# Optimization experiments

Measured on AMD Instinct MI355X. Metric: run time of the kernel, lower is better.

The kernel has to match this reference:

```python
import jax, jax.numpy as jnp
import numpy as np

HIDDEN = 2048
INTER = 8192
RETRIEVAL = 128
NUM_EXPERTS = 4096
NUM_KEYS = 64  # sqrt(NUM_EXPERTS)
TOP_K = 8
B, S = 4, 2048


def setup_inputs() -> dict:
    key = jax.random.key(0)
    ks = jax.random.split(key, 8)
    sc = 0.02
    return {
        "hidden_states": jax.random.normal(ks[0], (B, S, HIDDEN), jnp.float32),
        "W_q": jax.random.normal(ks[1], (HIDDEN, RETRIEVAL), jnp.float32) * sc,
        "keys": jax.random.normal(ks[2], (2, RETRIEVAL // 2, NUM_KEYS), jnp.float32) * sc,
        "down_embed": jax.random.normal(ks[3], (NUM_EXPERTS, HIDDEN), jnp.float32) * sc,
        "up_embed": jax.random.normal(ks[4], (NUM_EXPERTS, HIDDEN), jnp.float32) * sc,
        "gate_w": jax.random.normal(ks[5], (HIDDEN, INTER), jnp.float32) * sc,
        "up_w": jax.random.normal(ks[6], (HIDDEN, INTER), jnp.float32) * sc,
        "down_w": jax.random.normal(ks[7], (INTER, HIDDEN), jnp.float32) * sc,
    }


def reference(hidden_states, W_q, keys, down_embed, up_embed, gate_w, up_w, down_w):
    b, s, h = hidden_states.shape
    n = b * s
    # product-key routing (faithful to the source's view(2, N, -1) reshape)
    queries = (hidden_states @ W_q).reshape(2, n, RETRIEVAL // 2)  # [2, N, rd/2]
    routing = jnp.einsum('tnd,tdk->tnk', queries, keys)            # [2, N, num_keys]
    scores2, idx2 = jax.lax.top_k(routing, TOP_K)                  # [2, N, k]
    sx, sy = scores2[0], scores2[1]
    ix, iy = idx2[0], idx2[1]
    all_scores = (sx[:, :, None] + sy[:, None, :]).reshape(n, TOP_K * TOP_K)
    all_idx = (ix[:, :, None] * NUM_KEYS + iy[:, None, :]).reshape(n, TOP_K * TOP_K)
    scores, pk = jax.lax.top_k(all_scores, TOP_K)                  # [N, k]
    indices = jnp.take_along_axis(all_idx, pk, axis=-1)            # [N, k]
    # expert embedding gather + per-token tiny matmuls
    de = down_embed[indices]                                       # [N, k, H]
    ue = up_embed[indices]                                         # [N, k, H]
    x = hidden_states.reshape(n, h)
    ew = jnp.einsum('nh,nkh->nk', x, de)                           # [N, k]
    ew = jax.nn.silu(ew) * jax.nn.softmax(scores, axis=-1)
    experts_states = jnp.einsum('nk,nkh->nh', ew, ue).reshape(b, s, h)
    # dense SwiGLU MLP branch
    mlp = (jax.nn.silu(x @ gate_w) * (x @ up_w)) @ down_w
    return mlp.reshape(b, s, h) + experts_states
```

## Files before the change

### kernel.cpp

```cpp
#include <hip/hip_runtime.h>
#include <cstdint>
#include <cstddef>

#define HIDDEN 2048
#define INTER 8192
#define NTOK 8192
#define RET 128
#define NKEYS 64
#define TOPK 8

typedef __bf16 bf16_t;
typedef bf16_t bf16x8 __attribute__((ext_vector_type(8)));
typedef float floatx4 __attribute__((ext_vector_type(4)));

__device__ inline unsigned short f2bf(float f) {
  union { float f; unsigned u; } v; v.f = f;
  unsigned r = v.u + 0x7FFFu + ((v.u >> 16) & 1u);
  return (unsigned short)(r >> 16);
}
__device__ inline float bf2f(unsigned short s) {
  union { unsigned u; float f; } v; v.u = ((unsigned)s) << 16;
  return v.f;
}

__device__ inline void gld_lds16(unsigned short* lds, const unsigned short* g) {
  auto* l3 = reinterpret_cast<__attribute__((address_space(3))) unsigned int*>(
      reinterpret_cast<uintptr_t>(lds));
  auto* g1 = reinterpret_cast<const __attribute__((address_space(1))) unsigned int*>(
      reinterpret_cast<uintptr_t>(g));
  __builtin_amdgcn_global_load_lds(g1, l3, 16, 0, 0);
}

__device__ inline void xcd_map(int gx, int gy, int& bx, int& by) {
  if ((gx & 7) != 0) return;
  int lin = by * gx + bx;
  int W = gx >> 3;
  int xcd = lin & 7;
  int j = lin >> 3;
  int r = j / W, c = j % W;
  if (r & 1) c = W - 1 - c;
  bx = xcd * W + c;
  by = r;
}

__global__ __launch_bounds__(256) void cvt_bf16(const float* __restrict__ in,
                                                unsigned short* __restrict__ out,
                                                int count4) {
  for (int i = blockIdx.x * blockDim.x + threadIdx.x; i < count4;
       i += gridDim.x * blockDim.x) {
    float4 v = reinterpret_cast<const float4*>(in)[i];
    ushort4 o;
    o.x = f2bf(v.x); o.y = f2bf(v.y); o.z = f2bf(v.z); o.w = f2bf(v.w);
    reinterpret_cast<ushort4*>(out)[i] = o;
  }
}

__global__ __launch_bounds__(256) void transpose_cvt(const float* __restrict__ in,
                                                     unsigned short* __restrict__ out,
                                                     int R, int C) {
  __shared__ float tile[32][33];
  int c0 = blockIdx.x * 32, r0 = blockIdx.y * 32;
  int tx = threadIdx.x, ty = threadIdx.y;
#pragma unroll
  for (int it = 0; it < 4; ++it)
    tile[ty + it * 8][tx] = in[(size_t)(r0 + ty + it * 8) * C + c0 + tx];
  __syncthreads();
#pragma unroll
  for (int it = 0; it < 4; ++it)
    out[(size_t)(c0 + ty + it * 8) * R + r0 + tx] = f2bf(tile[tx][ty + it * 8]);
}

enum { EPI_F32 = 0, EPI_ADDF32 = 3 };

template <int MODE>
__global__ __launch_bounds__(256) void gemm_bt(const unsigned short* __restrict__ A,
                                               const unsigned short* __restrict__ B,
                                               float* __restrict__ Cf,
                                               int M, int N, int K) {
  __shared__ unsigned short As[128 * 64];
  __shared__ unsigned short Bs[128 * 64];
  const int tid = threadIdx.x;
  const int lane = tid & 63, wid = tid >> 6;
  const int wm = wid >> 1, wn = wid & 1;
  int bx = blockIdx.x, by = blockIdx.y;
  xcd_map(gridDim.x, gridDim.y, bx, by);
  const int m0 = by * 128, n0 = bx * 128;
  const int lr = lane & 15, q = lane >> 4;
  const int swz = lr & 7;

  floatx4 acc[4][4];
#pragma unroll
  for (int i = 0; i < 4; ++i)
#pragma unroll
    for (int j = 0; j < 4; ++j) acc[i][j] = (floatx4){0.f, 0.f, 0.f, 0.f};

  for (int k0 = 0; k0 < K; k0 += 64) {
#pragma unroll
    for (int s = 0; s < 4; ++s) {
      int c = s * 256 + wid * 64 + lane;
      int row = c >> 3, cc = (c & 7) ^ (row & 7);
      gld_lds16(&As[(s * 256 + wid * 64) * 8],
                A + (size_t)(m0 + row) * K + k0 + cc * 8);
      gld_lds16(&Bs[(s * 256 + wid * 64) * 8],
                B + (size_t)(n0 + row) * K + k0 + cc * 8);
    }
    __syncthreads();
#pragma unroll
    for (int kc = 0; kc < 2; ++kc) {
      const int coff = ((kc * 4 + q) ^ swz) * 8;
      bf16x8 af[4], bfv[4];
#pragma unroll
      for (int t = 0; t < 4; ++t) {
        af[t] = *reinterpret_cast<const bf16x8*>(
            &As[(wm * 64 + t * 16 + lr) * 64 + coff]);
        bfv[t] = *reinterpret_cast<const bf16x8*>(
            &Bs[(wn * 64 + t * 16 + lr) * 64 + coff]);
      }
#pragma unroll
      for (int i = 0; i < 4; ++i)
#pragma unroll
        for (int j = 0; j < 4; ++j)
          acc[i][j] = __builtin_amdgcn_mfma_f32_16x16x32_bf16(af[i], bfv[j],
                                                              acc[i][j], 0, 0, 0);
    }
    __syncthreads();
  }

#pragma unroll
  for (int i = 0; i < 4; ++i) {
    int rbase = m0 + wm * 64 + i * 16 + q * 4;
#pragma unroll
    for (int j = 0; j < 4; ++j) {
      int col = n0 + wn * 64 + j * 16 + lr;
#pragma unroll
      for (int r = 0; r < 4; ++r) {
        size_t idx = (size_t)(rbase + r) * N + col;
        float v = acc[i][j][r];
        if (MODE == EPI_F32) Cf[idx] = v;
        else Cf[idx] = v + Cf[idx];
      }
    }
  }
}

__global__ __launch_bounds__(256, 2) void gemm_gateup(
    const unsigned short* __restrict__ A, const unsigned short* __restrict__ Bg,
    const unsigned short* __restrict__ Bu, unsigned short* __restrict__ H,
    int M, int N, int K) {
  __shared__ unsigned short As[128 * 64];
  __shared__ unsigned short Bgs[128 * 64];
  __shared__ unsigned short Bus[128 * 64];
  const int tid = threadIdx.x;
  const int lane = tid & 63, wid = tid >> 6;
  const int wm = wid >> 1, wn = wid & 1;
  int bx = blockIdx.x, by = blockIdx.y;
  xcd_map(gridDim.x, gridDim.y, bx, by);
  const int m0 = by * 128, n0 = bx * 128;
  const int lr = lane & 15, q = lane >> 4;
  const int swz = lr & 7;

  floatx4 accg[4][4], accu[4][4];
#pragma unroll
  for (int i = 0; i < 4; ++i)
#pragma unroll
    for (int j = 0; j < 4; ++j) {
      accg[i][j] = (floatx4){0.f, 0.f, 0.f, 0.f};
      accu[i][j] = (floatx4){0.f, 0.f, 0.f, 0.f};
    }

  for (int k0 = 0; k0 < K; k0 += 64) {
#pragma unroll
    for (int s = 0; s < 4; ++s) {
      int c = s * 256 + wid * 64 + lane;
      int row = c >> 3, cc = (c & 7) ^ (row & 7);
      size_t arow = (size_t)(m0 + row) * K + k0 + cc * 8;
      size_t brow = (size_t)(n0 + row) * K + k0 + cc * 8;
      gld_lds16(&As[(s * 256 + wid * 64) * 8], A + arow);
      gld_lds16(&Bgs[(s * 256 + wid * 64) * 8], Bg + brow);
      gld_lds16(&Bus[(s * 256 + wid * 64) * 8], Bu + brow);
    }
    __syncthreads();
#pragma unroll
    for (int kc = 0; kc < 2; ++kc) {
      const int coff = ((kc * 4 + q) ^ swz) * 8;
      bf16x8 af[4], bgf[4], buf[4];
#pragma unroll
      for (int t = 0; t < 4; ++t) {
        af[t] = *reinterpret_cast<const bf16x8*>(
            &As[(wm * 64 + t * 16 + lr) * 64 + coff]);
        bgf[t] = *reinterpret_cast<const bf16x8*>(
            &Bgs[(wn * 64 + t * 16 + lr) * 64 + coff]);
        buf[t] = *reinterpret_cast<const bf16x8*>(
            &Bus[(wn * 64 + t * 16 + lr) * 64 + coff]);
      }
#pragma unroll
      for (int i = 0; i < 4; ++i)
#pragma unroll
        for (int j = 0; j < 4; ++j) {
          accg[i][j] = __builtin_amdgcn_mfma_f32_16x16x32_bf16(af[i], bgf[j],
                                                               accg[i][j], 0, 0, 0);
          accu[i][j] = __builtin_amdgcn_mfma_f32_16x16x32_bf16(af[i], buf[j],
                                                               accu[i][j], 0, 0, 0);
        }
    }
    __syncthreads();
  }

#pragma unroll
  for (int i = 0; i < 4; ++i) {
    int rbase = m0 + wm * 64 + i * 16 + q * 4;
#pragma unroll
    for (int j = 0; j < 4; ++j) {
      int col = n0 + wn * 64 + j * 16 + lr;
#pragma unroll
      for (int r = 0; r < 4; ++r) {
        float g = accg[i][j][r];
        float h = (g / (1.f + __expf(-g))) * accu[i][j][r];
        H[(size_t)(rbase + r) * N + col] = f2bf(h);
      }
    }
  }
}

__global__ __launch_bounds__(256) void routing_kernel(const float* __restrict__ Q,
                                                      const float* __restrict__ keys,
                                                      int* __restrict__ topi,
                                                      float* __restrict__ topw) {
  __shared__ float k0s[64 * 64];
  __shared__ float k1s[64 * 64];
  for (int i = threadIdx.x; i < 64 * 64; i += 256) {
    k0s[i] = keys[i];
    k1s[i] = keys[64 * 64 + i];
  }
  __syncthreads();
  const int lane = threadIdx.x & 63, wid = threadIdx.x >> 6;
  const int gw = blockIdx.x * 4 + wid;
  const float NEG = -__builtin_inff();

  for (int n = gw; n < NTOK; n += 1024) {
    int cbase = (n & 1) * 64;
    float qx = Q[(size_t)(n >> 1) * RET + cbase + lane];
    float qy = Q[(size_t)(NTOK / 2 + (n >> 1)) * RET + cbase + lane];
    float rx = 0.f, ry = 0.f;
#pragma unroll 8
    for (int d = 0; d < 64; ++d) {
      rx += __shfl(qx, d) * k0s[d * 64 + lane];
      ry += __shfl(qy, d) * k1s[d * 64 + lane];
    }
    float mvx = rx, mvy = ry;
    float keptx = 0.f, kepty = 0.f;
    int keptix = 0, keptiy = 0;
#pragma unroll
    for (int a = 0; a < 8; ++a) {
      float v = mvx; int ii = lane;
#pragma unroll
      for (int off = 32; off; off >>= 1) {
        float ov = __shfl_xor(v, off); int oi = __shfl_xor(ii, off);
        if (ov > v || (ov == v && oi < ii)) { v = ov; ii = oi; }
      }
      if (lane == a) { keptx = v; keptix = ii; }
      if (lane == ii) mvx = NEG;
      float w = mvy; int jj = lane;
#pragma unroll
      for (int off = 32; off; off >>= 1) {
        float ow = __shfl_xor(w, off); int oj = __shfl_xor(jj, off);
        if (ow > w || (ow == w && oj < jj)) { w = ow; jj = oj; }
      }
      if (lane == a) { kepty = w; keptiy = jj; }
      if (lane == jj) mvy = NEG;
    }
    float sa = __shfl(keptx, lane >> 3), sb = __shfl(kepty, lane & 7);
    int ia = __shfl(keptix, lane >> 3), ib = __shfl(keptiy, lane & 7);
    float mv = sa + sb;
    int pe = ia * NKEYS + ib;
    float maxs = 0.f, denom = 0.f, kw = 0.f;
    int ke = 0;
#pragma unroll
    for (int a = 0; a < 8; ++a) {
      float v = mv; int pos = lane; int e = pe;
#pragma unroll
      for (int off = 32; off; off >>= 1) {
        float ov = __shfl_xor(v, off);
        int opos = __shfl_xor(pos, off);
        int oe = __shfl_xor(e, off);
        if (ov > v || (ov == v && opos < pos)) { v = ov; pos = opos; e = oe; }
      }
      if (a == 0) maxs = v;
      denom += __expf(v - maxs);
      if (lane == a) { kw = __expf(v - maxs); ke = e; }
      if (lane == pos) mv = NEG;
    }
    if (lane < 8) {
      topw[(size_t)n * 8 + lane] = kw / denom;
      topi[(size_t)n * 8 + lane] = ke;
    }
  }
}

__global__ __launch_bounds__(256) void expert_kernel(const float* __restrict__ X,
                                                     const float* __restrict__ de,
                                                     const float* __restrict__ ue,
                                                     const int* __restrict__ topi,
                                                     const float* __restrict__ topw,
                                                     float* __restrict__ out) {
  const int n = blockIdx.x, t = threadIdx.x;
  __shared__ float red[4];
  __shared__ float coef_s;
  __shared__ int eidx[8];
  __shared__ float ewt[8];
  if (t < 8) {
    eidx[t] = topi[(size_t)n * 8 + t];
    ewt[t] = topw[(size_t)n * 8 + t];
  }
  const float* x = X + (size_t)n * HIDDEN + t * 8;
  float4 x0 = *(const float4*)x, x1 = *(const float4*)(x + 4);
  float a0 = 0, a1 = 0, a2 = 0, a3 = 0, a4 = 0, a5 = 0, a6 = 0, a7 = 0;
  __syncthreads();
#pragma unroll
  for (int k = 0; k < 8; ++k) {
    const float* dr = de + (size_t)eidx[k] * HIDDEN + t * 8;
    float4 d0 = *(const float4*)dr, d1 = *(const float4*)(dr + 4);
    float p = x0.x * d0.x + x0.y * d0.y + x0.z * d0.z + x0.w * d0.w +
              x1.x * d1.x + x1.y * d1.y + x1.z * d1.z + x1.w * d1.w;
#pragma unroll
    for (int off = 32; off; off >>= 1) p += __shfl_xor(p, off);
    if ((t & 63) == 0) red[t >> 6] = p;
    __syncthreads();
    if (t == 0) {
      float s = red[0] + red[1] + red[2] + red[3];
      coef_s = (s / (1.f + expf(-s))) * ewt[k];
    }
    __syncthreads();
    float c = coef_s;
    const float* ur = ue + (size_t)eidx[k] * HIDDEN + t * 8;
    float4 u0 = *(const float4*)ur, u1 = *(const float4*)(ur + 4);
    a0 += c * u0.x; a1 += c * u0.y; a2 += c * u0.z; a3 += c * u0.w;
    a4 += c * u1.x; a5 += c * u1.y; a6 += c * u1.z; a7 += c * u1.w;
  }
  float* op = out + (size_t)n * HIDDEN + t * 8;
  *(float4*)op = make_float4(a0, a1, a2, a3);
  *(float4*)(op + 4) = make_float4(a4, a5, a6, a7);
}

extern "C" void kernel_launch(void* const* d_in, const int* in_sizes, int n_in,
                              void* d_out, int out_size, void* d_ws, size_t ws_size,
                              hipStream_t stream) {
  const float* X    = (const float*)d_in[0];
  const float* Wq   = (const float*)d_in[1];
  const float* keys = (const float*)d_in[2];
  const float* de   = (const float*)d_in[3];
  const float* ue   = (const float*)d_in[4];
  const float* Wg   = (const float*)d_in[5];
  const float* Wu   = (const float*)d_in[6];
  const float* Wd   = (const float*)d_in[7];
  float* out = (float*)d_out;

  char* ws = (char*)d_ws;
  size_t o = 0;
  unsigned short* xb  = (unsigned short*)(ws + o); o += (size_t)NTOK * HIDDEN * 2;
  unsigned short* wgt = (unsigned short*)(ws + o); o += (size_t)HIDDEN * INTER * 2;
  unsigned short* wut = (unsigned short*)(ws + o); o += (size_t)HIDDEN * INTER * 2;
  unsigned short* wdt = (unsigned short*)(ws + o); o += (size_t)HIDDEN * INTER * 2;
  unsigned short* hbuf= (unsigned short*)(ws + o); o += (size_t)NTOK * INTER * 2;
  unsigned short* wqt = (unsigned short*)(ws + o); o += (size_t)RET * HIDDEN * 2;
  float* Q            = (float*)(ws + o);          o += (size_t)NTOK * RET * 4;
  int* topi           = (int*)(ws + o);            o += (size_t)NTOK * TOPK * 4;
  float* topw         = (float*)(ws + o);          o += (size_t)NTOK * TOPK * 4;

  cvt_bf16<<<4096, 256, 0, stream>>>(X, xb, NTOK * HIDDEN / 4);
  transpose_cvt<<<dim3(INTER / 32, HIDDEN / 32), dim3(32, 8), 0, stream>>>(Wg, wgt, HIDDEN, INTER);
  transpose_cvt<<<dim3(INTER / 32, HIDDEN / 32), dim3(32, 8), 0, stream>>>(Wu, wut, HIDDEN, INTER);
  transpose_cvt<<<dim3(HIDDEN / 32, INTER / 32), dim3(32, 8), 0, stream>>>(Wd, wdt, INTER, HIDDEN);
  transpose_cvt<<<dim3(RET / 32, HIDDEN / 32), dim3(32, 8), 0, stream>>>(Wq, wqt, HIDDEN, RET);

  gemm_bt<EPI_F32><<<dim3(1, NTOK / 128), 256, 0, stream>>>(xb, wqt, Q,
                                                            NTOK, RET, HIDDEN);
  routing_kernel<<<256, 256, 0, stream>>>(Q, keys, topi, topw);
  expert_kernel<<<NTOK, 256, 0, stream>>>(X, de, ue, topi, topw, out);

  gemm_gateup<<<dim3(INTER / 128, NTOK / 128), 256, 0, stream>>>(
      xb, wgt, wut, hbuf, NTOK, INTER, HIDDEN);
  gemm_bt<EPI_ADDF32><<<dim3(HIDDEN / 128, NTOK / 128), 256, 0, stream>>>(
      hbuf, wdt, out, NTOK, HIDDEN, INTER);
}
```

Measured before the change: 1.573 ms.

## Replace big GEMMs with 256-tile multi-stage pipelined kernels and batch expert reductions

Replaces the gate/up and down-projection GEMMs with 512-thread kernels that use 256-row tiles, a 4-buffer LDS ring with loads issued three tiles ahead, split A/B staging interleaved with MFMA phases, explicit vmcnt waits and raised wave priority during MFMA. This is meant to hide global load latency and raise data reuse per block, at the cost of 128 KB of dynamic LDS and a hand-tuned barrier and wait schedule that is fragile. The expert kernel also batches all eight dot-product reductions into a single barrier instead of two barriers per expert, cutting synchronisation overhead.

```diff
diff --git a/kernel.cpp b/kernel.cpp
--- a/kernel.cpp
+++ b/kernel.cpp
@@ -13,14 +13,26 @@
 typedef bf16_t bf16x8 __attribute__((ext_vector_type(8)));
 typedef float floatx4 __attribute__((ext_vector_type(4)));
 
+#define BARRIER() asm volatile("s_barrier" ::: "memory")
+#define WAIT_LGKM0()                                     \
+  do {                                                   \
+    asm volatile("s_waitcnt lgkmcnt(0)" ::: "memory");   \
+    __builtin_amdgcn_sched_barrier(0);                   \
+  } while (0)
+#define WAIT_VM8() asm volatile("s_waitcnt vmcnt(8)" ::: "memory")
+#define WAIT_VM4() asm volatile("s_waitcnt vmcnt(4)" ::: "memory")
+#define WAIT_VM0() asm volatile("s_waitcnt vmcnt(0)" ::: "memory")
+
+__device__ inline void tile_end_wait(int rem) {
+  if (rem >= 3) WAIT_VM8();
+  else if (rem == 2) WAIT_VM4();
+  else if (rem == 1) WAIT_VM0();
+}
+
 __device__ inline unsigned short f2bf(float f) {
   union { float f; unsigned u; } v; v.f = f;
   unsigned r = v.u + 0x7FFFu + ((v.u >> 16) & 1u);
   return (unsigned short)(r >> 16);
-}
-__device__ inline float bf2f(unsigned short s) {
-  union { unsigned u; float f; } v; v.u = ((unsigned)s) << 16;
-  return v.f;
 }
 
 __device__ inline void gld_lds16(unsigned short* lds, const unsigned short* g) {
@@ -41,6 +53,25 @@
   if (r & 1) c = W - 1 - c;
   bx = xcd * W + c;
   by = r;
+}
+
+__device__ inline void stage_op256(unsigned short* ldsbuf, const unsigned short* g,
+                                   int rows0, int K, int kt, int tid, int wid) {
+#pragma unroll
+  for (int i = 0; i < 2; ++i) {
+    int c = i * 512 + tid;
+    int row = c >> 2;
+    int cc = (c & 3) ^ (row & 3) ^ ((row >> 2) & 3);
+    gld_lds16(ldsbuf + (size_t)(i * 512 + wid * 64) * 8,
+              g + (size_t)(rows0 + row) * K + kt + cc * 8);
+  }
+}
+__device__ inline void stage_op128(unsigned short* ldsbuf, const unsigned short* g,
+                                   int rows0, int K, int kt, int tid, int wid) {
+  int row = tid >> 2;
+  int cc = (tid & 3) ^ (row & 3) ^ ((row >> 2) & 3);
+  gld_lds16(ldsbuf + (size_t)(wid * 64) * 8,
+            g + (size_t)(rows0 + row) * K + kt + cc * 8);
 }
 
 __global__ __launch_bounds__(256) void cvt_bf16(const float* __restrict__ in,
@@ -143,21 +174,123 @@
   }
 }
 
-__global__ __launch_bounds__(256, 2) void gemm_gateup(
-    const unsigned short* __restrict__ A, const unsigned short* __restrict__ Bg,
-    const unsigned short* __restrict__ Bu, unsigned short* __restrict__ H,
-    int M, int N, int K) {
-  __shared__ unsigned short As[128 * 64];
-  __shared__ unsigned short Bgs[128 * 64];
-  __shared__ unsigned short Bus[128 * 64];
+template <int MODE>
+__global__ __launch_bounds__(512, 2) void gemm256(const unsigned short* __restrict__ A,
+                                                  const unsigned short* __restrict__ B,
+                                                  float* __restrict__ Cf,
+                                                  int N, int K) {
+  extern __shared__ unsigned short sm[];
+  const int tid = threadIdx.x;
+  const int lane = tid & 63, wid = tid >> 6;
+  const int wm = wid >> 2, wn = wid & 3;
+  int bx = blockIdx.x, by = blockIdx.y;
+  xcd_map(gridDim.x, gridDim.y, bx, by);
+  const int m0 = by * 256, n0 = bx * 256;
+  const int lr = lane & 15, q = lane >> 4;
+  const int swz = (lr & 3) ^ ((lr >> 2) & 3);
+  const int coff = (q ^ swz) * 8;
+  unsigned short* Abase = sm;
+  unsigned short* Bbase = sm + 32768;
+  const int NT = K >> 5;
+
+  floatx4 acc[8][4];
+#pragma unroll
+  for (int i = 0; i < 8; ++i)
+#pragma unroll
+    for (int j = 0; j < 4; ++j) acc[i][j] = (floatx4){0.f, 0.f, 0.f, 0.f};
+
+#pragma unroll
+  for (int tt = 0; tt < 3; ++tt) {
+    stage_op256(Abase + tt * 8192, A, m0, K, tt * 32, tid, wid);
+    stage_op256(Bbase + tt * 8192, B, n0, K, tt * 32, tid, wid);
+  }
+  WAIT_VM8();
+  BARRIER();
+
+  for (int t = 0; t < NT; ++t) {
+    const int buf = t & 3;
+    const unsigned short* As = Abase + buf * 8192;
+    const unsigned short* Bs = Bbase + buf * 8192;
+    bf16x8 af[4], bfv[4];
+#pragma unroll
+    for (int m = 0; m < 4; ++m)
+      af[m] = *reinterpret_cast<const bf16x8*>(
+          &As[(wm * 128 + m * 16 + lr) * 32 + coff]);
+#pragma unroll
+    for (int n = 0; n < 4; ++n)
+      bfv[n] = *reinterpret_cast<const bf16x8*>(
+          &Bs[(wn * 64 + n * 16 + lr) * 32 + coff]);
+    if (t + 3 < NT)
+      stage_op256(Abase + ((t + 3) & 3) * 8192, A, m0, K, (t + 3) * 32, tid, wid);
+    BARRIER();
+    WAIT_LGKM0();
+    __builtin_amdgcn_s_setprio(1);
+#pragma unroll
+    for (int m = 0; m < 4; ++m)
+#pragma unroll
+      for (int n = 0; n < 4; ++n)
+        acc[m][n] = __builtin_amdgcn_mfma_f32_16x16x32_bf16(af[m], bfv[n],
+                                                            acc[m][n], 0, 0, 0);
+    __builtin_amdgcn_s_setprio(0);
+    __builtin_amdgcn_sched_barrier(0);
+    BARRIER();
+#pragma unroll
+    for (int m = 0; m < 4; ++m)
+      af[m] = *reinterpret_cast<const bf16x8*>(
+          &As[(wm * 128 + (m + 4) * 16 + lr) * 32 + coff]);
+    if (t + 3 < NT)
+      stage_op256(Bbase + ((t + 3) & 3) * 8192, B, n0, K, (t + 3) * 32, tid, wid);
+    BARRIER();
+    WAIT_LGKM0();
+    __builtin_amdgcn_s_setprio(1);
+#pragma unroll
+    for (int m = 0; m < 4; ++m)
+#pragma unroll
+      for (int n = 0; n < 4; ++n)
+        acc[m + 4][n] = __builtin_amdgcn_mfma_f32_16x16x32_bf16(af[m], bfv[n],
+                                                                acc[m + 4][n], 0, 0, 0);
+    __builtin_amdgcn_s_setprio(0);
+    __builtin_amdgcn_sched_barrier(0);
+    tile_end_wait(NT - 1 - t);
+    BARRIER();
+  }
+
+#pragma unroll
+  for (int m = 0; m < 8; ++m) {
+    int rbase = m0 + wm * 128 + m * 16 + q * 4;
+#pragma unroll
+    for (int n = 0; n < 4; ++n) {
+      int col = n0 + wn * 64 + n * 16 + lr;
+#pragma unroll
+      for (int r = 0; r < 4; ++r) {
+        size_t idx = (size_t)(rbase + r) * N + col;
+        float v = acc[m][n][r];
+        if (MODE == EPI_F32) Cf[idx] = v;
+        else Cf[idx] = v + Cf[idx];
+      }
+    }
+  }
+}
+
+__global__ __launch_bounds__(512, 2) void gateup256(const unsigned short* __restrict__ A,
+                                                    const unsigned short* __restrict__ Bg,
+                                                    const unsigned short* __restrict__ Bu,
+                                                    unsigned short* __restrict__ H,
+                                                    int N, int K) {
+  extern __shared__ unsigned short sm[];
   const int tid = threadIdx.x;
   const int lane = tid & 63, wid = tid >> 6;
   const int wm = wid >> 1, wn = wid & 1;
   int bx = blockIdx.x, by = blockIdx.y;
   xcd_map(gridDim.x, gridDim.y, bx, by);
-  const int m0 = by * 128, n0 = bx * 128;
+  const int m0 = by * 256, n0 = bx * 128;
   const int lr = lane & 15, q = lane >> 4;
-  const int swz = lr & 7;
+  const int swz = (lr & 3) ^ ((lr >> 2) & 3);
+  const int coff = (q ^ swz) * 8;
+  unsigned short* Abase = sm;
+  unsigned short* Bgbase = sm + 32768;
+  unsigned short* Bubase = sm + 49152;
+  const int NT = K >> 5;
 
   floatx4 accg[4][4], accu[4][4];
 #pragma unroll
@@ -168,54 +301,85 @@
       accu[i][j] = (floatx4){0.f, 0.f, 0.f, 0.f};
     }
 
-  for (int k0 = 0; k0 < K; k0 += 64) {
-#pragma unroll
-    for (int s = 0; s < 4; ++s) {
-      int c = s * 256 + wid * 64 + lane;
-      int row = c >> 3, cc = (c & 7) ^ (row & 7);
-      size_t arow = (size_t)(m0 + row) * K + k0 + cc * 8;
-      size_t brow = (size_t)(n0 + row) * K + k0 + cc * 8;
-      gld_lds16(&As[(s * 256 + wid * 64) * 8], A + arow);
-      gld_lds16(&Bgs[(s * 256 + wid * 64) * 8], Bg + brow);
-      gld_lds16(&Bus[(s * 256 + wid * 64) * 8], Bu + brow);
-    }
-    __syncthreads();
-#pragma unroll
-    for (int kc = 0; kc < 2; ++kc) {
-      const int coff = ((kc * 4 + q) ^ swz) * 8;
-      bf16x8 af[4], bgf[4], buf[4];
-#pragma unroll
-      for (int t = 0; t < 4; ++t) {
-        af[t] = *reinterpret_cast<const bf16x8*>(
-            &As[(wm * 64 + t * 16 + lr) * 64 + coff]);
-        bgf[t] = *reinterpret_cast<const bf16x8*>(
-            &Bgs[(wn * 64 + t * 16 + lr) * 64 + coff]);
-        buf[t] = *reinterpret_cast<const bf16x8*>(
-            &Bus[(wn * 64 + t * 16 + lr) * 64 + coff]);
-      }
-#pragma unroll
-      for (int i = 0; i < 4; ++i)
-#pragma unroll
-        for (int j = 0; j < 4; ++j) {
-          accg[i][j] = __builtin_amdgcn_mfma_f32_16x16x32_bf16(af[i], bgf[j],
-                                                               accg[i][j], 0, 0, 0);
-          accu[i][j] = __builtin_amdgcn_mfma_f32_16x16x32_bf16(af[i], buf[j],
-                                                               accu[i][j], 0, 0, 0);
-        }
-    }
-    __syncthreads();
-  }
-
-#pragma unroll
-  for (int i = 0; i < 4; ++i) {
-    int rbase = m0 + wm * 64 + i * 16 + q * 4;
-#pragma unroll
-    for (int j = 0; j < 4; ++j) {
-      int col = n0 + wn * 64 + j * 16 + lr;
+#pragma unroll
+  for (int tt = 0; tt < 3; ++tt) {
+    stage_op256(Abase + tt * 8192, A, m0, K, tt * 32, tid, wid);
+    stage_op128(Bgbase + tt * 4096, Bg, n0, K, tt * 32, tid, wid);
+    stage_op128(Bubase + tt * 4096, Bu, n0, K, tt * 32, tid, wid);
+  }
+  WAIT_VM8();
+  BARRIER();
+
+  for (int t = 0; t < NT; ++t) {
+    const int buf = t & 3;
+    const unsigned short* As = Abase + buf * 8192;
+    const unsigned short* Bgs = Bgbase + buf * 4096;
+    const unsigned short* Bus = Bubase + buf * 4096;
+    bf16x8 af[2], bg[4], bu[4];
+#pragma unroll
+    for (int m = 0; m < 2; ++m)
+      af[m] = *reinterpret_cast<const bf16x8*>(
+          &As[(wm * 64 + m * 16 + lr) * 32 + coff]);
+#pragma unroll
+    for (int n = 0; n < 4; ++n) {
+      bg[n] = *reinterpret_cast<const bf16x8*>(
+          &Bgs[(wn * 64 + n * 16 + lr) * 32 + coff]);
+      bu[n] = *reinterpret_cast<const bf16x8*>(
+          &Bus[(wn * 64 + n * 16 + lr) * 32 + coff]);
+    }
+    if (t + 3 < NT)
+      stage_op256(Abase + ((t + 3) & 3) * 8192, A, m0, K, (t + 3) * 32, tid, wid);
+    BARRIER();
+    WAIT_LGKM0();
+    __builtin_amdgcn_s_setprio(1);
+#pragma unroll
+    for (int m = 0; m < 2; ++m)
+#pragma unroll
+      for (int n = 0; n < 4; ++n) {
+        accg[m][n] = __builtin_amdgcn_mfma_f32_16x16x32_bf16(af[m], bg[n],
+                                                             accg[m][n], 0, 0, 0);
+        accu[m][n] = __builtin_amdgcn_mfma_f32_16x16x32_bf16(af[m], bu[n],
+                                                             accu[m][n], 0, 0, 0);
+      }
+    __builtin_amdgcn_s_setprio(0);
+    __builtin_amdgcn_sched_barrier(0);
+    BARRIER();
+#pragma unroll
+    for (int m = 0; m < 2; ++m)
+      af[m] = *reinterpret_cast<const bf16x8*>(
+          &As[(wm * 64 + (m + 2) * 16 + lr) * 32 + coff]);
+    if (t + 3 < NT) {
+      stage_op128(Bgbase + ((t + 3) & 3) * 4096, Bg, n0, K, (t + 3) * 32, tid, wid);
+      stage_op128(Bubase + ((t + 3) & 3) * 4096, Bu, n0, K, (t + 3) * 32, tid, wid);
+    }
+    BARRIER();
+    WAIT_LGKM0();
+    __builtin_amdgcn_s_setprio(1);
+#pragma unroll
+    for (int m = 0; m < 2; ++m)
+#pragma unroll
+      for (int n = 0; n < 4; ++n) {
+        accg[m + 2][n] = __builtin_amdgcn_mfma_f32_16x16x32_bf16(af[m], bg[n],
+                                                                 accg[m + 2][n], 0, 0, 0);
+        accu[m + 2][n] = __builtin_amdgcn_mfma_f32_16x16x32_bf16(af[m], bu[n],
+                                                                 accu[m + 2][n], 0, 0, 0);
+      }
+    __builtin_amdgcn_s_setprio(0);
+    __builtin_amdgcn_sched_barrier(0);
+    tile_end_wait(NT - 1 - t);
+    BARRIER();
+  }
+
+#pragma unroll
+  for (int m = 0; m < 4; ++m) {
+    int rbase = m0 + wm * 64 + m * 16 + q * 4;
+#pragma unroll
+    for (int n = 0; n < 4; ++n) {
+      int col = n0 + wn * 64 + n * 16 + lr;
 #pragma unroll
       for (int r = 0; r < 4; ++r) {
-        float g = accg[i][j][r];
-        float h = (g / (1.f + __expf(-g))) * accu[i][j][r];
+        float g = accg[m][n][r];
+        float h = (g / (1.f + __expf(-g))) * accu[m][n][r];
         H[(size_t)(rbase + r) * N + col] = f2bf(h);
       }
     }
@@ -304,36 +468,46 @@
                                                      const float* __restrict__ topw,
                                                      float* __restrict__ out) {
   const int n = blockIdx.x, t = threadIdx.x;
-  __shared__ float red[4];
-  __shared__ float coef_s;
+  const int lane = t & 63, wid = t >> 6;
+  __shared__ float red[4][8];
   __shared__ int eidx[8];
   __shared__ float ewt[8];
   if (t < 8) {
     eidx[t] = topi[(size_t)n * 8 + t];
     ewt[t] = topw[(size_t)n * 8 + t];
   }
+  __syncthreads();
   const float* x = X + (size_t)n * HIDDEN + t * 8;
   float4 x0 = *(const float4*)x, x1 = *(const float4*)(x + 4);
-  float a0 = 0, a1 = 0, a2 = 0, a3 = 0, a4 = 0, a5 = 0, a6 = 0, a7 = 0;
-  __syncthreads();
+  float p[8];
 #pragma unroll
   for (int k = 0; k < 8; ++k) {
     const float* dr = de + (size_t)eidx[k] * HIDDEN + t * 8;
     float4 d0 = *(const float4*)dr, d1 = *(const float4*)(dr + 4);
-    float p = x0.x * d0.x + x0.y * d0.y + x0.z * d0.z + x0.w * d0.w +
-              x1.x * d1.x + x1.y * d1.y + x1.z * d1.z + x1.w * d1.w;
-#pragma unroll
-    for (int off = 32; off; off >>= 1) p += __shfl_xor(p, off);
-    if ((t & 63) == 0) red[t >> 6] = p;
-    __syncthreads();
-    if (t == 0) {
-      float s = red[0] + red[1] + red[2] + red[3];
-      coef_s = (s / (1.f + expf(-s))) * ewt[k];
-    }
-    __syncthreads();
-    float c = coef_s;
+    p[k] = x0.x * d0.x + x0.y * d0.y + x0.z * d0.z + x0.w * d0.w +
+           x1.x * d1.x + x1.y * d1.y + x1.z * d1.z + x1.w * d1.w;
+  }
+#pragma unroll
+  for (int k = 0; k < 8; ++k)
+#pragma unroll
+    for (int off = 32; off; off >>= 1) p[k] += __shfl_xor(p[k], off);
+  if (lane == 0) {
+#pragma unroll
+    for (int k = 0; k < 8; ++k) red[wid][k] = p[k];
+  }
+  __syncthreads();
+  float coef[8];
+#pragma unroll
+  for (int k = 0; k < 8; ++k) {
+    float s = red[0][k] + red[1][k] + red[2][k] + red[3][k];
+    coef[k] = (s / (1.f + __expf(-s))) * ewt[k];
+  }
+  float a0 = 0, a1 = 0, a2 = 0, a3 = 0, a4 = 0, a5 = 0, a6 = 0, a7 = 0;
+#pragma unroll
+  for (int k = 0; k < 8; ++k) {
     const float* ur = ue + (size_t)eidx[k] * HIDDEN + t * 8;
     float4 u0 = *(const float4*)ur, u1 = *(const float4*)(ur + 4);
+    float c = coef[k];
     a0 += c * u0.x; a1 += c * u0.y; a2 += c * u0.z; a3 += c * u0.w;
     a4 += c * u1.x; a5 += c * u1.y; a6 += c * u1.z; a7 += c * u1.w;
   }
@@ -367,6 +541,17 @@
   int* topi           = (int*)(ws + o);            o += (size_t)NTOK * TOPK * 4;
   float* topw         = (float*)(ws + o);          o += (size_t)NTOK * TOPK * 4;
 
+  static bool attr_done = false;
+  if (!attr_done) {
+    auto kd = gemm256<EPI_ADDF32>;
+    auto kg = gateup256;
+    (void)hipFuncSetAttribute(reinterpret_cast<const void*>(kd),
+                              hipFuncAttributeMaxDynamicSharedMemorySize, 131072);
+    (void)hipFuncSetAttribute(reinterpret_cast<const void*>(kg),
+                              hipFuncAttributeMaxDynamicSharedMemorySize, 131072);
+    attr_done = true;
+  }
+
   cvt_bf16<<<4096, 256, 0, stream>>>(X, xb, NTOK * HIDDEN / 4);
   transpose_cvt<<<dim3(INTER / 32, HIDDEN / 32), dim3(32, 8), 0, stream>>>(Wg, wgt, HIDDEN, INTER);
   transpose_cvt<<<dim3(INTER / 32, HIDDEN / 32), dim3(32, 8), 0, stream>>>(Wu, wut, HIDDEN, INTER);
@@ -378,8 +563,8 @@
   routing_kernel<<<256, 256, 0, stream>>>(Q, keys, topi, topw);
   expert_kernel<<<NTOK, 256, 0, stream>>>(X, de, ue, topi, topw, out);
 
-  gemm_gateup<<<dim3(INTER / 128, NTOK / 128), 256, 0, stream>>>(
-      xb, wgt, wut, hbuf, NTOK, INTER, HIDDEN);
-  gemm_bt<EPI_ADDF32><<<dim3(HIDDEN / 128, NTOK / 128), 256, 0, stream>>>(
-      hbuf, wdt, out, NTOK, HIDDEN, INTER);
-}
+  gateup256<<<dim3(INTER / 128, NTOK / 256), 512, 131072, stream>>>(
+      xb, wgt, wut, hbuf, INTER, HIDDEN);
+  gemm256<EPI_ADDF32><<<dim3(HIDDEN / 256, NTOK / 256), 512, 131072, stream>>>(
+      hbuf, wdt, out, HIDDEN, INTER);
+}
```

New measurement: 1.563 ms. About the same (-0.6%).
